# Optimization experiments

Hardware: AMD Instinct MI355X
Metric: run time of the kernel (lower is better)

Reference implementation:

```python
import jax, jax.numpy as jnp
import numpy as np
from jax import lax

B = 1024
T = 32           # length_sec = 384 // (2*2*3*1)
HGT = 7          # height_image = 28 // (1*2*2*1)
CC = 32          # last conv channels
AD = HGT * CC    # abstract_dim = 224
HID = 256        # attention decoder hidden
VOCAB = 29
OUT_LEN = 25


def setup_inputs() -> dict:
    ks = jax.random.split(jax.random.key(0), 24)
    n = lambda k, s, sc=1.0: jax.random.normal(k, s, jnp.float32) * sc
    return {
        "x": n(ks[0], (B, 1, 384, 28)),
        "conv1_w": n(ks[1], (4, 1, 3, 3), 0.2),   "conv1_b": n(ks[2], (4,), 0.1),
        "conv2_w": n(ks[3], (16, 4, 3, 3), 0.2),  "conv2_b": n(ks[4], (16,), 0.1),
        "conv3_w": n(ks[5], (16, 16, 3, 3), 0.2), "conv3_b": n(ks[6], (16,), 0.1),
        "conv4_w": n(ks[7], (32, 16, 3, 3), 0.2), "conv4_b": n(ks[8], (32,), 0.1),
        "h0": n(ks[9], (1, AD)), "c0": n(ks[10], (1, AD)),
        "lstm_Wih": n(ks[11], (4 * AD, AD), 0.05), "lstm_Whh": n(ks[12], (4 * AD, AD), 0.05),
        "lstm_bih": n(ks[13], (4 * AD,), 0.05),    "lstm_bhh": n(ks[14], (4 * AD,), 0.05),
        "att_w": n(ks[15], (1, HID + AD), 0.05),   "att_b": n(ks[16], (1,), 0.05),
        "dec_Wih": n(ks[17], (4 * HID, AD), 0.05), "dec_Whh": n(ks[18], (4 * HID, HID), 0.05),
        "dec_bih": n(ks[19], (4 * HID,), 0.05),    "dec_bhh": n(ks[20], (4 * HID,), 0.05),
        "out_w": n(ks[21], (VOCAB, HID), 0.05),    "out_b": n(ks[22], (VOCAB,), 0.05),
    }


def _lstm_cell(h, c, xt, Wih, Whh, bih, bhh):
    # PyTorch gate order: i, f, g, o
    g = xt @ Wih.T + bih + h @ Whh.T + bhh
    i, f, gg, o = jnp.split(g, 4, axis=-1)
    c = jax.nn.sigmoid(f) * c + jax.nn.sigmoid(i) * jnp.tanh(gg)
    h = jax.nn.sigmoid(o) * jnp.tanh(c)
    return h, c


def reference(x, conv1_w, conv1_b, conv2_w, conv2_b, conv3_w, conv3_b, conv4_w, conv4_b,
              h0, c0, lstm_Wih, lstm_Whh, lstm_bih, lstm_bhh,
              att_w, att_b, dec_Wih, dec_Whh, dec_bih, dec_bhh, out_w, out_b):
    def crp(z, w, b, pool):
        y = lax.conv_general_dilated(z, w, (1, 1), [(1, 1), (1, 1)],
                                     dimension_numbers=('NCHW', 'OIHW', 'NCHW'))
        y = jax.nn.relu(y + b[None, :, None, None])
        win = (1, 1) + pool
        return lax.reduce_window(y, -jnp.inf, lax.max, win, win, 'VALID')

    y1 = crp(x, conv1_w, conv1_b, (2, 1))
    y2 = crp(y1, conv2_w, conv2_b, (2, 2))
    y3 = crp(y2, conv3_w, conv3_b, (3, 2))
    y4 = crp(y3, conv4_w, conv4_b, (1, 1))          # [B, 32, 32, 7]
    Bsz = x.shape[0]
    # y5[b,t,i] = y4[b, i%32, t, i//32]  ==  transpose + reshape (replaces python loop)
    y5 = jnp.transpose(y4, (0, 2, 3, 1)).reshape(Bsz, T, AD)   # [B, T, 224]

    # encoder LSTM (seq-major scan, like torch LSTM)
    def estep(carry, xt):
        h, c = carry
        h, c = _lstm_cell(h, c, xt, lstm_Wih, lstm_Whh, lstm_bih, lstm_bhh)
        return (h, c), h
    h0b = jnp.tile(h0, (Bsz, 1))
    c0b = jnp.tile(c0, (Bsz, 1))
    _, hs = lax.scan(estep, (h0b, c0b), jnp.transpose(y5, (1, 0, 2)))
    y8 = jnp.transpose(hs, (1, 0, 2))                # [B, T, 224]

    # attention decoder: additive score softmax(linear(concat(h, enc)))
    w_h = att_w[0, :HID]     # hidden part
    w_e = att_w[0, HID:]     # encoder part
    enc_score = y8 @ w_e     # [B, T], precomputed once

    def dstep(carry, _):
        h, c = carry
        scores = enc_score + (h @ w_h)[:, None] + att_b[0]      # [B, T]
        alpha = jax.nn.softmax(scores, axis=1)
        ctx = jnp.einsum('bt,btd->bd', alpha, y8)               # [B, 224]
        h, c = _lstm_cell(h, c, ctx, dec_Wih, dec_Whh, dec_bih, dec_bhh)
        return (h, c), h @ out_w.T + out_b                      # [B, 29]

    hdec = jnp.zeros((Bsz, HID), x.dtype)
    _, outs = lax.scan(dstep, (hdec, hdec), None, length=OUT_LEN)  # [25, B, 29]
    return jnp.transpose(outs, (1, 2, 0))            # [B, 29, 25]
```

## Files before the change

### kernel.cpp

```cpp
#include <hip/hip_runtime.h>

typedef unsigned short u16;
typedef unsigned int u32;
typedef unsigned long long u64;
typedef __bf16 bfrag __attribute__((ext_vector_type(8)));
typedef float v4f __attribute__((ext_vector_type(4)));

#define DI __device__ __forceinline__

DI float bf2f(u16 b){ union{u32 u; float f;} c; c.u = ((u32)b)<<16; return c.f; }
DI u16 f2bf(float f){ union{float f; u32 u;} c; c.f=f; u32 u=c.u; return (u16)((u + 0x7FFFu + ((u>>16)&1u))>>16); }
DI float sigm(float x){ return 1.0f/(1.0f+__expf(-x)); }
DI float tanhf_(float x){ float a=fabsf(x); float e=__expf(2.0f*a); float r=1.0f-2.0f/(e+1.0f); return x<0.0f? -r : r; }

DI void cvt_one(const float* __restrict__ src, u16* __restrict__ hi, u16* __restrict__ lo, u32 i){
  float v = src[i]; u16 h = f2bf(v); hi[i] = h; lo[i] = f2bf(v - bf2f(h));
}
__global__ __launch_bounds__(256) void k_cvt4(const float* __restrict__ s0, u16* __restrict__ h0p, u16* __restrict__ l0p,
                                              const float* __restrict__ s1, u16* __restrict__ h1p, u16* __restrict__ l1p,
                                              const float* __restrict__ s2, u16* __restrict__ h2p, u16* __restrict__ l2p,
                                              const float* __restrict__ s3, u16* __restrict__ h3p, u16* __restrict__ l3p,
                                              u32* __restrict__ ef){
  u32 b = blockIdx.x, tid = threadIdx.x;
  if (b < 784u)            cvt_one(s0, h0p, l0p, b*256u + tid);
  else if (b < 1568u)      cvt_one(s1, h1p, l1p, (b-784u)*256u + tid);
  else if (b < 2464u)      cvt_one(s2, h2p, l2p, (b-1568u)*256u + tid);
  else if (b < 3488u)      cvt_one(s3, h3p, l3p, (b-2464u)*256u + tid);
  else {
    #pragma unroll
    for (int j=0;j<4;j++) ef[(u32)j*256u + tid] = 0u;
  }
}

__global__ __launch_bounds__(256) void k_conv1(const float* __restrict__ x, const float* __restrict__ w,
                                               const float* __restrict__ bias, float* __restrict__ y1q, u32 bbase){
  u32 gid = blockIdx.x*256u + threadIdx.x;
  u32 bl = gid/768u, r = gid - bl*768u;
  u32 oy = r>>2, xg = r&3u;
  const float* xb = x + (u64)(bbase+bl)*10752u;
  float win[4][9];
  #pragma unroll
  for (int rr=0; rr<4; rr++){
    int iy = 2*(int)oy - 1 + rr;
    bool vy = (u32)iy < 384u;
    #pragma unroll
    for (int cc=0; cc<9; cc++){
      int ix = (int)(xg*7u) + cc - 1;
      win[rr][cc] = (vy && (u32)ix < 28u) ? xb[iy*28 + ix] : 0.0f;
    }
  }
  #pragma unroll
  for (int co=0; co<4; co++){
    float wf[9];
    #pragma unroll
    for (int j=0;j<9;j++) wf[j] = w[co*9+j];
    float bc = bias[co];
    float* outp = y1q + ((u64)(bl*4u+co)*192u + oy)*28u + xg*7u;
    #pragma unroll
    for (int ox=0; ox<7; ox++){
      float m = 0.0f;
      #pragma unroll
      for (int py=0; py<2; py++){
        float s = bc;
        #pragma unroll
        for (int dy=0; dy<3; dy++)
          #pragma unroll
          for (int dx=0; dx<3; dx++)
            s += win[py+dy][ox+dx]*wf[dy*3+dx];
        m = fmaxf(m, s);
      }
      outp[ox] = m;
    }
  }
}

__global__ __launch_bounds__(256) void k_conv2(const float* __restrict__ y1q, const float* __restrict__ w,
                                               const float* __restrict__ bias, float* __restrict__ y2q){
  u32 gid = blockIdx.x*256u + threadIdx.x;
  u32 bl = gid/1536u, r = gid - bl*1536u;
  u32 oy = r>>4, xg = (r>>3)&1u, cp = r&7u;
  const float* inb = y1q + (u64)bl*21504u;
  float acc[2][7][4];
  #pragma unroll
  for (int c2=0;c2<2;c2++)
    #pragma unroll
    for (int i=0;i<7;i++){ acc[c2][i][0]=0.f;acc[c2][i][1]=0.f;acc[c2][i][2]=0.f;acc[c2][i][3]=0.f; }
  for (int ci=0; ci<4; ci++){
    float win[4][16];
    const float* pl = inb + ci*5376;
    #pragma unroll
    for (int rr=0; rr<4; rr++){
      int iy = 2*(int)oy - 1 + rr;
      bool vy = (u32)iy < 192u;
      #pragma unroll
      for (int cc=0; cc<16; cc++){
        int ix = (int)(xg*14u) + cc - 1;
        win[rr][cc] = (vy && (u32)ix<28u) ? pl[iy*28+ix] : 0.0f;
      }
    }
    float wf[2][9];
    #pragma unroll
    for (int c2=0;c2<2;c2++)
      #pragma unroll
      for (int j=0;j<9;j++) wf[c2][j] = w[((cp*2u+(u32)c2)*4u+(u32)ci)*9u+j];
    #pragma unroll
    for (int c2=0;c2<2;c2++)
      #pragma unroll
      for (int ol=0; ol<7; ol++)
        #pragma unroll
        for (int py=0; py<2; py++)
          #pragma unroll
          for (int px=0; px<2; px++){
            float s = acc[c2][ol][py*2+px];
            #pragma unroll
            for (int dy=0; dy<3; dy++)
              #pragma unroll
              for (int dx=0; dx<3; dx++)
                s += win[py+dy][2*ol+px+dx]*wf[c2][dy*3+dx];
            acc[c2][ol][py*2+px] = s;
          }
  }
  #pragma unroll
  for (int c2=0;c2<2;c2++){
    u32 co = cp*2u+(u32)c2;
    float bc = bias[co];
    float* outp = y2q + ((u64)(bl*16u+co)*96u + oy)*14u + xg*7u;
    #pragma unroll
    for (int ol=0; ol<7; ol++){
      float m = fmaxf(fmaxf(acc[c2][ol][0],acc[c2][ol][1]), fmaxf(acc[c2][ol][2],acc[c2][ol][3])) + bc;
      outp[ol] = fmaxf(m, 0.0f);
    }
  }
}

__global__ __launch_bounds__(256) void k_conv3(const float* __restrict__ y2q, const float* __restrict__ w,
                                               const float* __restrict__ bias, float* __restrict__ y3, u32 bbase){
  u32 gid = blockIdx.x*256u + threadIdx.x;
  u32 bl = gid/512u, r = gid - bl*512u;
  u32 oy = r>>4, co = r&15u;
  const float* inb = y2q + (u64)bl*21504u;
  float acc[7][6];
  #pragma unroll
  for (int i=0;i<7;i++){
    #pragma unroll
    for (int j=0;j<6;j++) acc[i][j]=0.0f;
  }
  for (int ci=0; ci<16; ci++){
    float win[5][16];
    const float* pl = inb + ci*1344;
    #pragma unroll
    for (int rr=0; rr<5; rr++){
      int iy = 3*(int)oy - 1 + rr;
      bool vy = (u32)iy < 96u;
      #pragma unroll
      for (int cc=0; cc<16; cc++){
        int ix = cc-1;
        win[rr][cc] = (vy && (u32)ix<14u) ? pl[iy*14+ix] : 0.0f;
      }
    }
    float wf[9];
    #pragma unroll
    for (int j=0;j<9;j++) wf[j] = w[((u32)co*16u+(u32)ci)*9u+j];
    #pragma unroll
    for (int ox=0; ox<7; ox++){
      #pragma unroll
      for (int py=0; py<3; py++)
        #pragma unroll
        for (int px=0; px<2; px++){
          float s = acc[ox][py*2+px];
          #pragma unroll
          for (int dy=0; dy<3; dy++)
            #pragma unroll
            for (int dx=0; dx<3; dx++)
              s += win[py+dy][2*ox+px+dx]*wf[dy*3+dx];
          acc[ox][py*2+px] = s;
        }
    }
  }
  float bc = bias[co];
  float* outp = y3 + ((u64)((bbase+bl)*16u+co)*32u + oy)*7u;
  #pragma unroll
  for (int ox=0; ox<7; ox++){
    float m = acc[ox][0];
    #pragma unroll
    for (int j=1;j<6;j++) m = fmaxf(m, acc[ox][j]);
    outp[ox] = fmaxf(m + bc, 0.0f);
  }
}

__global__ __launch_bounds__(256) void k_conv4(const float* __restrict__ y3, const float* __restrict__ w,
                                               const float* __restrict__ bias, float* __restrict__ y5){
  u32 gid = blockIdx.x*256u + threadIdx.x;
  u32 b = gid/512u, r = gid - b*512u;
  u32 oy = r>>4, cp = r&15u;
  u32 co0 = cp*2u;
  const float* inb = y3 + (u64)b*3584u;
  float acc[2][7];
  #pragma unroll
  for (int i=0;i<2;i++){
    #pragma unroll
    for (int j=0;j<7;j++) acc[i][j]=0.0f;
  }
  for (int ci=0; ci<16; ci++){
    float win[3][9];
    const float* pl = inb + ci*224;
    #pragma unroll
    for (int rr=0; rr<3; rr++){
      int iy = (int)oy - 1 + rr;
      bool vy = (u32)iy < 32u;
      #pragma unroll
      for (int cc=0; cc<9; cc++){
        int ix = cc-1;
        win[rr][cc] = (vy && (u32)ix<7u) ? pl[iy*7+ix] : 0.0f;
      }
    }
    #pragma unroll
    for (int c2=0; c2<2; c2++){
      float wf[9];
      #pragma unroll
      for (int j=0;j<9;j++) wf[j] = w[((co0+(u32)c2)*16u+(u32)ci)*9u+j];
      #pragma unroll
      for (int ox=0; ox<7; ox++){
        float s = acc[c2][ox];
        #pragma unroll
        for (int dy=0; dy<3; dy++)
          #pragma unroll
          for (int dx=0; dx<3; dx++)
            s += win[dy][ox+dx]*wf[dy*3+dx];
        acc[c2][ox] = s;
      }
    }
  }
  #pragma unroll
  for (int c2=0; c2<2; c2++){
    float bc = bias[co0+(u32)c2];
    #pragma unroll
    for (int ox=0; ox<7; ox++)
      y5[((u64)b*32u + oy)*224u + (u32)ox*32u + (co0+(u32)c2)] = fmaxf(acc[c2][ox] + bc, 0.0f);
  }
}

__global__ __launch_bounds__(1024) void k_zero(u32* __restrict__ p){
  p[threadIdx.x] = 0u;
}

__global__ __launch_bounds__(512, 4) void k_enc7(const u16* __restrict__ WihHi, const u16* __restrict__ WihLo,
                                                 const u16* __restrict__ WhhHi, const u16* __restrict__ WhhLo,
                                                 const float* __restrict__ bih, const float* __restrict__ bhh,
                                                 const float* __restrict__ y5, const float* __restrict__ h0,
                                                 const float* __restrict__ c0, float* __restrict__ y8,
                                                 u32* __restrict__ eflags){
  __shared__ __align__(16) u16 Ahi[16*456], Alo[16*456];
  __shared__ __align__(16) float gsh[16*132];
  __shared__ __align__(16) float bsh[128];
  u32 tid = threadIdx.x, w = tid>>6, lane = tid&63u, nl = lane&15u, quad = lane>>4;
  u32 bid = blockIdx.x, g = bid & 63u, q = bid >> 6;
  u32 b0 = g*16u, hc0 = q*32u;
  if (tid < 128u){
    u32 gi = tid>>5, col = gi*224u + hc0 + (tid&31u);
    bsh[tid] = bih[col] + bhh[col];
  }
  for (u32 it=tid; it<3584u; it+=512u){
    u32 r = it/224u, c = it - r*224u;
    float v = h0[c]; u16 hb = f2bf(v);
    Ahi[r*456u+224u+c] = hb; Alo[r*456u+224u+c] = f2bf(v - bf2f(hb));
  }
  float creg = c0[hc0 + (tid&31u)];
  u32* fE = eflags + g*16u;
  const u32 col = (w>>1)*224u + hc0 + (w&1u)*16u + nl;
  const u32 gl  = (w>>1)*32u  + (w&1u)*16u + nl;
  __syncthreads();
  for (u32 t=0; t<32u; t++){
    #pragma unroll
    for (int i=0;i<7;i++){
      u32 item = (u32)i*512u + tid;
      u32 r = item/224u, c = item - r*224u;
      float v = y5[((u64)(b0+r)*32u + t)*224u + c];
      u16 hb = f2bf(v);
      Ahi[r*456u+c] = hb; Alo[r*456u+c] = f2bf(v - bf2f(hb));
    }
    __syncthreads();
    v4f acc = {};
    #pragma unroll
    for (int kt=0; kt<14; kt++){
      u32 ka = (u32)kt*32u + quad*8u;
      bfrag ah = *(const bfrag*)&Ahi[nl*456u + ka];
      bfrag al = *(const bfrag*)&Alo[nl*456u + ka];
      bfrag bh, bl;
      if (kt<7){
        u64 o = (u64)col*224u + ka;
        bh = *(const bfrag*)&WihHi[o]; bl = *(const bfrag*)&WihLo[o];
      } else {
        u64 o = (u64)col*224u + (ka - 224u);
        bh = *(const bfrag*)&WhhHi[o]; bl = *(const bfrag*)&WhhLo[o];
      }
      acc = __builtin_amdgcn_mfma_f32_16x16x32_bf16(ah, bh, acc, 0,0,0);
      acc = __builtin_amdgcn_mfma_f32_16x16x32_bf16(al, bh, acc, 0,0,0);
      acc = __builtin_amdgcn_mfma_f32_16x16x32_bf16(ah, bl, acc, 0,0,0);
    }
    #pragma unroll
    for (int rg=0; rg<4; rg++)
      gsh[(quad*4u+(u32)rg)*132u + gl] = acc[rg];
    __syncthreads();
    {
      u32 row = tid>>5, hl = tid&31u;
      float gi_ = gsh[row*132u +       hl] + bsh[hl];
      float gf_ = gsh[row*132u + 32u + hl] + bsh[32u+hl];
      float gg_ = gsh[row*132u + 64u + hl] + bsh[64u+hl];
      float go_ = gsh[row*132u + 96u + hl] + bsh[96u+hl];
      float cv = sigm(gf_)*creg + sigm(gi_)*tanhf_(gg_);
      float hv = sigm(go_)*tanhf_(cv);
      creg = cv;
      union{float f; u32 u;} cu; cu.f = hv;
      __hip_atomic_store((u32*)&y8[((u64)(b0+row)*32u + t)*224u + hc0 + hl], cu.u,
                         __ATOMIC_RELAXED, __HIP_MEMORY_SCOPE_AGENT);
    }
    __syncthreads();
    if (tid==0u)
      __hip_atomic_fetch_add(fE, 1u, __ATOMIC_RELEASE, __HIP_MEMORY_SCOPE_AGENT);
    if (t < 31u){
      if (tid==0u){
        while (__hip_atomic_load(fE, __ATOMIC_RELAXED, __HIP_MEMORY_SCOPE_AGENT) < 7u*(t+1u))
          __builtin_amdgcn_s_sleep(2);
      }
      __syncthreads();
      for (u32 it=tid; it<3584u; it+=512u){
        u32 r = it/224u, c = it - r*224u;
        u32 uv = __hip_atomic_load((const u32*)&y8[((u64)(b0+r)*32u + t)*224u + c],
                                   __ATOMIC_RELAXED, __HIP_MEMORY_SCOPE_AGENT);
        union{u32 u; float f;} cu; cu.u = uv;
        u16 hb = f2bf(cu.f);
        Ahi[r*456u+224u+c] = hb; Alo[r*456u+224u+c] = f2bf(cu.f - bf2f(hb));
      }
    }
  }
}

__global__ __launch_bounds__(512) void k_dec4(const float* __restrict__ y8,
    const float* __restrict__ attw, const float* __restrict__ attb,
    const u16* __restrict__ WihHi, const u16* __restrict__ WihLo,
    const u16* __restrict__ WhhHi, const u16* __restrict__ WhhLo,
    const float* __restrict__ bih, const float* __restrict__ bhh,
    u32* __restrict__ hist, u32* __restrict__ ctxc, u32* __restrict__ flags){
  __shared__ __align__(16) u16 Ahi[16*488], Alo[16*488];
  __shared__ __align__(16) float hfull[16*256];
  __shared__ __align__(16) float gsh[16*260];
  __shared__ __align__(16) float esc[16*33];
  __shared__ __align__(16) float alp[16*33];
  __shared__ __align__(16) float bsh[256];
  u32 tid=threadIdx.x, w=tid>>6, lane=tid&63u, nl=lane&15u, quad=lane>>4;
  u32 p = blockIdx.x, xcd = p&7u, slot = p>>3;
  u32 q = xcd>>1;
  u32 g = (xcd&1u)*32u + slot;
  u32 b0 = g*16u, hc0 = q*64u;
  for (u32 it=tid; it<256u; it+=512u){
    u32 gi = it>>6, col = gi*256u + hc0 + (it&63u);
    bsh[it] = bih[col] + bhh[col];
  }
  for (u32 it=tid; it<4096u; it+=512u){
    u32 r=it>>8, c=it&255u;
    Ahi[r*488u+224u+c]=0; Alo[r*488u+224u+c]=0;
    hfull[it]=0.0f;
  }
  {
    u32 r=tid>>5, t=tid&31u;
    const float* yr = y8 + ((u64)(b0+r)*32u + t)*224u;
    const float* we = attw + 256;
    float sacc=0.0f;
    #pragma unroll 8
    for (int j=0;j<224;j++) sacc += yr[j]*we[j];
    esc[r*33u+t] = sacc + attb[0];
  }
  float cst[2] = {0.0f, 0.0f};
  u32* fh = flags + g*16u;
  u32* fc = flags + g*16u + 8u;
  const u32 nt0 = w, nt1 = w + 8u;
  const u32 col0 = (nt0>>2)*256u + hc0 + (nt0&3u)*16u + nl;
  const u32 col1 = (nt1>>2)*256u + hc0 + (nt1&3u)*16u + nl;
  const u32 gl0  = (nt0>>2)*64u + (nt0&3u)*16u + nl;
  const u32 gl1  = (nt1>>2)*64u + (nt1&3u)*16u + nl;
  __syncthreads();
  for (u32 s=0; s<25u; s++){
    if (s>0u){
      if (tid==0u){
        while (__hip_atomic_load(fh, __ATOMIC_RELAXED, __HIP_MEMORY_SCOPE_AGENT) < 4u*s)
          __builtin_amdgcn_s_sleep(2);
      }
      __syncthreads();
      u32* hrow = hist + ((u64)(s-1u)*1024u + b0)*256u;
      for (u32 it=tid; it<4096u; it+=512u){
        u32 v = __hip_atomic_load(&hrow[it], __ATOMIC_RELAXED, __HIP_MEMORY_SCOPE_AGENT);
        u32 r = it>>8, c = it&255u;
        u16 hb = (u16)(v>>16), lb = (u16)(v&0xFFFFu);
        Ahi[r*488u+224u+c] = hb; Alo[r*488u+224u+c] = lb;
        hfull[it] = bf2f(hb) + bf2f(lb);
      }
      __syncthreads();
    }
    {
      u32 r=tid>>5, t=tid&31u;
      float part=0.0f;
      if (s>0u){
        #pragma unroll
        for (int qq=0; qq<8; qq++){
          u32 c = t + (u32)qq*32u;
          part += hfull[r*256u+c]*attw[c];
        }
        #pragma unroll
        for (int off=16; off; off>>=1) part += __shfl_xor(part, off, 32);
      }
      float sv = esc[r*33u+t] + part;
      float mx = sv;
      #pragma unroll
      for (int off=16; off; off>>=1) mx = fmaxf(mx, __shfl_xor(mx, off, 32));
      float e = __expf(sv-mx);
      float ssum = e;
      #pragma unroll
      for (int off=16; off; off>>=1) ssum += __shfl_xor(ssum, off, 32);
      alp[r*33u+t] = e/ssum;
    }
    __syncthreads();
    u32* cdst = ctxc + (u64)(s&1u)*229376u + (u64)g*3584u;
    for (u32 it=tid; it<896u; it+=512u){
      u32 rr = it/56u, cc = it - rr*56u + q*56u;
      const float* yb = y8 + (u64)(b0+rr)*32u*224u + cc;
      float a0=0.0f;
      #pragma unroll
      for (int tt=0; tt<32; tt++) a0 += alp[rr*33u+(u32)tt]*yb[(u32)tt*224u];
      u16 hb = f2bf(a0), lb = f2bf(a0 - bf2f(hb));
      __hip_atomic_store(&cdst[rr*224u+cc], ((u32)hb<<16)|(u32)lb, __ATOMIC_RELAXED, __HIP_MEMORY_SCOPE_AGENT);
    }
    __syncthreads();
    if (tid==0u){
      __hip_atomic_fetch_add(fc, 1u, __ATOMIC_RELEASE, __HIP_MEMORY_SCOPE_AGENT);
      while (__hip_atomic_load(fc, __ATOMIC_RELAXED, __HIP_MEMORY_SCOPE_AGENT) < 4u*(s+1u))
        __builtin_amdgcn_s_sleep(2);
    }
    __syncthreads();
    for (u32 it=tid; it<3584u; it+=512u){
      u32 v = __hip_atomic_load(&cdst[it], __ATOMIC_RELAXED, __HIP_MEMORY_SCOPE_AGENT);
      u32 rr = it/224u, cc = it - rr*224u;
      Ahi[rr*488u+cc] = (u16)(v>>16); Alo[rr*488u+cc] = (u16)(v&0xFFFFu);
    }
    __syncthreads();
    v4f acc0 = {}, acc1 = {};
    #pragma unroll
    for (int kt=0; kt<15; kt++){
      u32 ka = (u32)kt*32u + quad*8u;
      bfrag afh = *(const bfrag*)&Ahi[nl*488u + ka];
      bfrag afl = *(const bfrag*)&Alo[nl*488u + ka];
      bfrag b0h, b0l, b1h, b1l;
      if (kt<7){
        u64 o0 = (u64)col0*224u + ka, o1 = (u64)col1*224u + ka;
        b0h = *(const bfrag*)&WihHi[o0]; b0l = *(const bfrag*)&WihLo[o0];
        b1h = *(const bfrag*)&WihHi[o1]; b1l = *(const bfrag*)&WihLo[o1];
      } else {
        u32 kb = ka - 224u;
        u64 o0 = (u64)col0*256u + kb, o1 = (u64)col1*256u + kb;
        b0h = *(const bfrag*)&WhhHi[o0]; b0l = *(const bfrag*)&WhhLo[o0];
        b1h = *(const bfrag*)&WhhHi[o1]; b1l = *(const bfrag*)&WhhLo[o1];
      }
      acc0 = __builtin_amdgcn_mfma_f32_16x16x32_bf16(afh, b0h, acc0, 0,0,0);
      acc0 = __builtin_amdgcn_mfma_f32_16x16x32_bf16(afl, b0h, acc0, 0,0,0);
      acc0 = __builtin_amdgcn_mfma_f32_16x16x32_bf16(afh, b0l, acc0, 0,0,0);
      acc1 = __builtin_amdgcn_mfma_f32_16x16x32_bf16(afh, b1h, acc1, 0,0,0);
      acc1 = __builtin_amdgcn_mfma_f32_16x16x32_bf16(afl, b1h, acc1, 0,0,0);
      acc1 = __builtin_amdgcn_mfma_f32_16x16x32_bf16(afh, b1l, acc1, 0,0,0);
    }
    #pragma unroll
    for (int rg=0; rg<4; rg++){
      gsh[(quad*4u+(u32)rg)*260u + gl0] = acc0[rg];
      gsh[(quad*4u+(u32)rg)*260u + gl1] = acc1[rg];
    }
    __syncthreads();
    u32* hdst = hist + ((u64)s*1024u + b0)*256u + hc0;
    #pragma unroll
    for (int k2=0; k2<2; k2++){
      u32 l = (u32)k2*512u + tid;
      u32 row = l>>6, hl = l&63u;
      float gi_ = gsh[row*260u + hl]         + bsh[hl];
      float gf_ = gsh[row*260u + 64u  + hl]  + bsh[64u+hl];
      float gg_ = gsh[row*260u + 128u + hl]  + bsh[128u+hl];
      float go_ = gsh[row*260u + 192u + hl]  + bsh[192u+hl];
      float cv = sigm(gf_)*cst[k2] + sigm(gi_)*tanhf_(gg_);
      float hv = sigm(go_)*tanhf_(cv);
      cst[k2] = cv;
      u16 hb = f2bf(hv), lb = f2bf(hv - bf2f(hb));
      __hip_atomic_store(&hdst[row*256u + hl], ((u32)hb<<16)|(u32)lb, __ATOMIC_RELAXED, __HIP_MEMORY_SCOPE_AGENT);
    }
    __syncthreads();
    if (tid==0u)
      __hip_atomic_fetch_add(fh, 1u, __ATOMIC_RELEASE, __HIP_MEMORY_SCOPE_AGENT);
  }
}

__global__ __launch_bounds__(256) void k_out(const u32* __restrict__ hist, const float* __restrict__ outw,
                                             const float* __restrict__ outb, float* __restrict__ outp){
  __shared__ __align__(16) float wsh[29*260];
  __shared__ __align__(16) float hrow[256];
  u32 tid = threadIdx.x, b = blockIdx.x;
  for (u32 it=tid; it<7424u; it+=256u){
    u32 v = it/256u, c = it&255u;
    wsh[v*260u+c] = outw[v*256u+c];
  }
  __syncthreads();
  for (u32 s=0; s<25u; s++){
    u32 v = hist[((u64)s*1024u + b)*256u + tid];
    hrow[tid] = bf2f((u16)(v>>16)) + bf2f((u16)(v&0xFFFFu));
    __syncthreads();
    if (tid < 232u){
      u32 vv = tid>>3, k8 = tid&7u;
      float a = 0.0f;
      #pragma unroll
      for (int j=0;j<32;j++) a += hrow[k8*32u+(u32)j]*wsh[vv*260u + k8*32u + (u32)j];
      #pragma unroll
      for (int off=4; off; off>>=1) a += __shfl_xor(a, off, 8);
      if (k8==0u) outp[((u64)b*29u + vv)*25u + s] = a + outb[vv];
    }
    __syncthreads();
  }
}

extern "C" void kernel_launch(void* const* d_in, const int* in_sizes, int n_in,
                              void* d_out, int out_size, void* d_ws, size_t ws_size,
                              hipStream_t stream){
  (void)in_sizes; (void)n_in; (void)out_size; (void)ws_size;
  const float* x    = (const float*)d_in[0];
  const float* c1w  = (const float*)d_in[1];
  const float* c1b  = (const float*)d_in[2];
  const float* c2w  = (const float*)d_in[3];
  const float* c2b  = (const float*)d_in[4];
  const float* c3w  = (const float*)d_in[5];
  const float* c3b  = (const float*)d_in[6];
  const float* c4w  = (const float*)d_in[7];
  const float* c4b  = (const float*)d_in[8];
  const float* h0   = (const float*)d_in[9];
  const float* c0   = (const float*)d_in[10];
  const float* lWih = (const float*)d_in[11];
  const float* lWhh = (const float*)d_in[12];
  const float* lbih = (const float*)d_in[13];
  const float* lbhh = (const float*)d_in[14];
  const float* attw = (const float*)d_in[15];
  const float* attb = (const float*)d_in[16];
  const float* dWih = (const float*)d_in[17];
  const float* dWhh = (const float*)d_in[18];
  const float* dbih = (const float*)d_in[19];
  const float* dbhh = (const float*)d_in[20];
  const float* outw = (const float*)d_in[21];
  const float* outb = (const float*)d_in[22];
  float* out = (float*)d_out;
  char* ws = (char*)d_ws;
  float* y1q = (float*)(ws);
  float* y2q = (float*)(ws + 22020096ull);
  float* y3  = (float*)(ws + 44040192ull);
  float* y5  = (float*)(ws);
  float* y8  = (float*)(ws + 29360128ull);
  u32* hist  = (u32*)(ws);
  u32* ctxc  = (u32*)(ws + 26214400ull);
  u32* flags = (u32*)(ws + 28049408ull);
  u16* lWihHi = (u16*)(ws + 58720256ull);
  u16* lWihLo = (u16*)(ws + 59121664ull);
  u16* lWhhHi = (u16*)(ws + 59523072ull);
  u16* lWhhLo = (u16*)(ws + 59924480ull);
  u16* dWihHi = (u16*)(ws + 60325888ull);
  u16* dWihLo = (u16*)(ws + 60784640ull);
  u16* dWhhHi = (u16*)(ws + 61243392ull);
  u16* dWhhLo = (u16*)(ws + 61767680ull);
  u32* eflags = (u32*)d_out;

  k_cvt4<<<dim3(3489), dim3(256), 0, stream>>>(lWih, lWihHi, lWihLo,
                                               lWhh, lWhhHi, lWhhLo,
                                               dWih, dWihHi, dWihLo,
                                               dWhh, dWhhHi, dWhhLo, eflags);
  for (u32 q=0; q<4; q++){
    k_conv1<<<dim3(768),  dim3(256), 0, stream>>>(x, c1w, c1b, y1q, q*256u);
    k_conv2<<<dim3(1536), dim3(256), 0, stream>>>(y1q, c2w, c2b, y2q);
    k_conv3<<<dim3(512),  dim3(256), 0, stream>>>(y2q, c3w, c3b, y3, q*256u);
  }
  k_conv4<<<dim3(2048), dim3(256), 0, stream>>>(y3, c4w, c4b, y5);
  k_enc7 <<<dim3(448), dim3(512), 0, stream>>>(lWihHi, lWihLo, lWhhHi, lWhhLo, lbih, lbhh,
                                               y5, h0, c0, y8, eflags);
  k_zero <<<dim3(1), dim3(1024), 0, stream>>>(flags);
  k_dec4 <<<dim3(256), dim3(512), 0, stream>>>(y8, attw, attb, dWihHi, dWihLo, dWhhHi, dWhhLo,
                                               dbih, dbhh, hist, ctxc, flags);
  k_out  <<<dim3(1024), dim3(256), 0, stream>>>(hist, outw, outb, out);
}
```

Baseline: 2.009 ms.

## Fuse four conv-relu-pool stages into one per-sample kernel using LDS

Replaces the four separate conv kernels, which were launched per quarter batch, with a single kernel where each block handles one sample. Intermediate activations and all conv weights are kept in shared memory, and conv1/conv2 are processed in row strips. This removes the large global round-trips of intermediate activations and most kernel launches. In exchange, the large shared-memory footprint limits each CU to one 256-thread block, reducing latency hiding, and conv1/conv2 now use scalar shared-memory loops with per-element bounds checks.

Result: slower. 4.446 ms (+121.3%).

```diff
diff --git a/kernel.cpp b/kernel.cpp
--- a/kernel.cpp
+++ b/kernel.cpp
@@ -32,211 +32,177 @@
   }
 }
 
-__global__ __launch_bounds__(256) void k_conv1(const float* __restrict__ x, const float* __restrict__ w,
-                                               const float* __restrict__ bias, float* __restrict__ y1q, u32 bbase){
-  u32 gid = blockIdx.x*256u + threadIdx.x;
-  u32 bl = gid/768u, r = gid - bl*768u;
-  u32 oy = r>>2, xg = r&3u;
-  const float* xb = x + (u64)(bbase+bl)*10752u;
-  float win[4][9];
-  #pragma unroll
-  for (int rr=0; rr<4; rr++){
-    int iy = 2*(int)oy - 1 + rr;
-    bool vy = (u32)iy < 384u;
-    #pragma unroll
-    for (int cc=0; cc<9; cc++){
-      int ix = (int)(xg*7u) + cc - 1;
-      win[rr][cc] = (vy && (u32)ix < 28u) ? xb[iy*28 + ix] : 0.0f;
-    }
-  }
-  #pragma unroll
-  for (int co=0; co<4; co++){
-    float wf[9];
-    #pragma unroll
-    for (int j=0;j<9;j++) wf[j] = w[co*9+j];
-    float bc = bias[co];
-    float* outp = y1q + ((u64)(bl*4u+co)*192u + oy)*28u + xg*7u;
-    #pragma unroll
-    for (int ox=0; ox<7; ox++){
+__global__ __launch_bounds__(256, 1) void k_convf(const float* __restrict__ x,
+    const float* __restrict__ c1w, const float* __restrict__ c1b,
+    const float* __restrict__ c2w, const float* __restrict__ c2b,
+    const float* __restrict__ c3w, const float* __restrict__ c3b,
+    const float* __restrict__ c4w, const float* __restrict__ c4b,
+    float* __restrict__ y5){
+  __shared__ __align__(16) float wsh[7592];
+  __shared__ __align__(16) float y2s[21504];
+  __shared__ __align__(16) float y1s[2016];
+  __shared__ __align__(16) float y3s[3584];
+  u32 tid = threadIdx.x, b = blockIdx.x;
+  const float* xb = x + (u64)b*10752u;
+  for (u32 it=tid; it<576u;  it+=256u) wsh[it]        = c2w[it];
+  for (u32 it=tid; it<2304u; it+=256u) wsh[576u+it]   = c3w[it];
+  for (u32 it=tid; it<4608u; it+=256u) wsh[2880u+it]  = c4w[it];
+  if (tid < 36u) wsh[7556u+tid] = c1w[tid];
+  if (tid < 4u)  wsh[7488u+tid] = c1b[tid];
+  if (tid < 16u) wsh[7492u+tid] = c2b[tid];
+  if (tid < 16u) wsh[7508u+tid] = c3b[tid];
+  if (tid < 32u) wsh[7524u+tid] = c4b[tid];
+  __syncthreads();
+  for (u32 s=0; s<12u; s++){
+    for (u32 it=tid; it<2016u; it+=256u){
+      u32 ch = it/504u, rem = it - ch*504u;
+      u32 j = rem/28u, c = rem - j*28u;
+      int gr = 16*(int)s - 1 + (int)j;
       float m = 0.0f;
-      #pragma unroll
-      for (int py=0; py<2; py++){
-        float s = bc;
-        #pragma unroll
-        for (int dy=0; dy<3; dy++)
+      if ((u32)gr < 192u){
+        float bc = wsh[7488u+ch];
+        #pragma unroll
+        for (int py=0; py<2; py++){
+          float a = bc;
           #pragma unroll
-          for (int dx=0; dx<3; dx++)
-            s += win[py+dy][ox+dx]*wf[dy*3+dx];
-        m = fmaxf(m, s);
-      }
-      outp[ox] = m;
-    }
-  }
-}
-
-__global__ __launch_bounds__(256) void k_conv2(const float* __restrict__ y1q, const float* __restrict__ w,
-                                               const float* __restrict__ bias, float* __restrict__ y2q){
-  u32 gid = blockIdx.x*256u + threadIdx.x;
-  u32 bl = gid/1536u, r = gid - bl*1536u;
-  u32 oy = r>>4, xg = (r>>3)&1u, cp = r&7u;
-  const float* inb = y1q + (u64)bl*21504u;
-  float acc[2][7][4];
-  #pragma unroll
-  for (int c2=0;c2<2;c2++)
-    #pragma unroll
-    for (int i=0;i<7;i++){ acc[c2][i][0]=0.f;acc[c2][i][1]=0.f;acc[c2][i][2]=0.f;acc[c2][i][3]=0.f; }
-  for (int ci=0; ci<4; ci++){
-    float win[4][16];
-    const float* pl = inb + ci*5376;
-    #pragma unroll
-    for (int rr=0; rr<4; rr++){
-      int iy = 2*(int)oy - 1 + rr;
-      bool vy = (u32)iy < 192u;
-      #pragma unroll
-      for (int cc=0; cc<16; cc++){
-        int ix = (int)(xg*14u) + cc - 1;
-        win[rr][cc] = (vy && (u32)ix<28u) ? pl[iy*28+ix] : 0.0f;
-      }
-    }
-    float wf[2][9];
-    #pragma unroll
-    for (int c2=0;c2<2;c2++)
-      #pragma unroll
-      for (int j=0;j<9;j++) wf[c2][j] = w[((cp*2u+(u32)c2)*4u+(u32)ci)*9u+j];
-    #pragma unroll
-    for (int c2=0;c2<2;c2++)
-      #pragma unroll
-      for (int ol=0; ol<7; ol++)
+          for (int dy=0; dy<3; dy++){
+            int iy = 2*gr + py - 1 + dy;
+            bool vy = (u32)iy < 384u;
+            #pragma unroll
+            for (int dx=0; dx<3; dx++){
+              int ix = (int)c - 1 + dx;
+              a += (vy && (u32)ix < 28u) ? xb[iy*28+ix]*wsh[7556u+ch*9u+(u32)(dy*3+dx)] : 0.0f;
+            }
+          }
+          m = fmaxf(m, a);
+        }
+      }
+      y1s[it] = m;
+    }
+    __syncthreads();
+    for (u32 it=tid; it<1792u; it+=256u){
+      u32 co = it/112u, rem = it - co*112u;
+      u32 r = rem/14u, ox = rem - r*14u;
+      float a0=0.f, a1=0.f, a2=0.f, a3=0.f;
+      #pragma unroll
+      for (int ci=0; ci<4; ci++){
+        const float* wp = &wsh[(co*4u+(u32)ci)*9u];
         #pragma unroll
         for (int py=0; py<2; py++)
           #pragma unroll
           for (int px=0; px<2; px++){
-            float s = acc[c2][ol][py*2+px];
+            float sacc = (py==0) ? (px==0 ? a0 : a1) : (px==0 ? a2 : a3);
+            #pragma unroll
+            for (int dy=0; dy<3; dy++){
+              u32 lr = 2u*r + (u32)(py+dy);
+              #pragma unroll
+              for (int dx=0; dx<3; dx++){
+                int lc = 2*(int)ox + px - 1 + dx;
+                sacc += ((u32)lc < 28u) ? y1s[(u32)ci*504u + lr*28u + (u32)lc]*wp[dy*3+dx] : 0.0f;
+              }
+            }
+            if (py==0){ if (px==0) a0=sacc; else a1=sacc; } else { if (px==0) a2=sacc; else a3=sacc; }
+          }
+      }
+      float m = fmaxf(fmaxf(a0,a1), fmaxf(a2,a3)) + wsh[7492u+co];
+      y2s[co*1344u + (8u*s+r)*14u + ox] = fmaxf(m, 0.0f);
+    }
+    __syncthreads();
+  }
+  for (u32 it=tid; it<512u; it+=256u){
+    u32 co = it>>5, oy = it&31u;
+    float acc[7][6];
+    #pragma unroll
+    for (int i=0;i<7;i++){
+      #pragma unroll
+      for (int j=0;j<6;j++) acc[i][j]=0.0f;
+    }
+    for (int ci=0; ci<16; ci++){
+      float win[5][16];
+      #pragma unroll
+      for (int rr=0; rr<5; rr++){
+        int iy = 3*(int)oy - 1 + rr;
+        bool vy = (u32)iy < 96u;
+        #pragma unroll
+        for (int cc=0; cc<16; cc++){
+          int ix = cc-1;
+          win[rr][cc] = (vy && (u32)ix<14u) ? y2s[(u32)ci*1344u + (u32)iy*14u + (u32)ix] : 0.0f;
+        }
+      }
+      float wf[9];
+      #pragma unroll
+      for (int j=0;j<9;j++) wf[j] = wsh[576u + (co*16u+(u32)ci)*9u + (u32)j];
+      #pragma unroll
+      for (int ox=0; ox<7; ox++){
+        #pragma unroll
+        for (int py=0; py<3; py++)
+          #pragma unroll
+          for (int px=0; px<2; px++){
+            float sacc = acc[ox][py*2+px];
             #pragma unroll
             for (int dy=0; dy<3; dy++)
               #pragma unroll
               for (int dx=0; dx<3; dx++)
-                s += win[py+dy][2*ol+px+dx]*wf[c2][dy*3+dx];
-            acc[c2][ol][py*2+px] = s;
+                sacc += win[py+dy][2*ox+px+dx]*wf[dy*3+dx];
+            acc[ox][py*2+px] = sacc;
           }
-  }
-  #pragma unroll
-  for (int c2=0;c2<2;c2++){
-    u32 co = cp*2u+(u32)c2;
-    float bc = bias[co];
-    float* outp = y2q + ((u64)(bl*16u+co)*96u + oy)*14u + xg*7u;
-    #pragma unroll
-    for (int ol=0; ol<7; ol++){
-      float m = fmaxf(fmaxf(acc[c2][ol][0],acc[c2][ol][1]), fmaxf(acc[c2][ol][2],acc[c2][ol][3])) + bc;
-      outp[ol] = fmaxf(m, 0.0f);
-    }
-  }
-}
-
-__global__ __launch_bounds__(256) void k_conv3(const float* __restrict__ y2q, const float* __restrict__ w,
-                                               const float* __restrict__ bias, float* __restrict__ y3, u32 bbase){
-  u32 gid = blockIdx.x*256u + threadIdx.x;
-  u32 bl = gid/512u, r = gid - bl*512u;
-  u32 oy = r>>4, co = r&15u;
-  const float* inb = y2q + (u64)bl*21504u;
-  float acc[7][6];
-  #pragma unroll
-  for (int i=0;i<7;i++){
-    #pragma unroll
-    for (int j=0;j<6;j++) acc[i][j]=0.0f;
-  }
-  for (int ci=0; ci<16; ci++){
-    float win[5][16];
-    const float* pl = inb + ci*1344;
-    #pragma unroll
-    for (int rr=0; rr<5; rr++){
-      int iy = 3*(int)oy - 1 + rr;
-      bool vy = (u32)iy < 96u;
-      #pragma unroll
-      for (int cc=0; cc<16; cc++){
-        int ix = cc-1;
-        win[rr][cc] = (vy && (u32)ix<14u) ? pl[iy*14+ix] : 0.0f;
-      }
-    }
-    float wf[9];
-    #pragma unroll
-    for (int j=0;j<9;j++) wf[j] = w[((u32)co*16u+(u32)ci)*9u+j];
+      }
+    }
+    float bc = wsh[7508u+co];
     #pragma unroll
     for (int ox=0; ox<7; ox++){
-      #pragma unroll
-      for (int py=0; py<3; py++)
-        #pragma unroll
-        for (int px=0; px<2; px++){
-          float s = acc[ox][py*2+px];
+      float m = acc[ox][0];
+      #pragma unroll
+      for (int j=1;j<6;j++) m = fmaxf(m, acc[ox][j]);
+      y3s[co*224u + oy*7u + (u32)ox] = fmaxf(m + bc, 0.0f);
+    }
+  }
+  __syncthreads();
+  for (u32 it=tid; it<512u; it+=256u){
+    u32 oy = it>>4, cp = it&15u;
+    u32 co0 = cp*2u;
+    float acc[2][7];
+    #pragma unroll
+    for (int i=0;i<2;i++){
+      #pragma unroll
+      for (int j=0;j<7;j++) acc[i][j]=0.0f;
+    }
+    for (int ci=0; ci<16; ci++){
+      float win[3][9];
+      #pragma unroll
+      for (int rr=0; rr<3; rr++){
+        int iy = (int)oy - 1 + rr;
+        bool vy = (u32)iy < 32u;
+        #pragma unroll
+        for (int cc=0; cc<9; cc++){
+          int ix = cc-1;
+          win[rr][cc] = (vy && (u32)ix<7u) ? y3s[(u32)ci*224u + (u32)iy*7u + (u32)ix] : 0.0f;
+        }
+      }
+      #pragma unroll
+      for (int c2=0; c2<2; c2++){
+        float wf[9];
+        #pragma unroll
+        for (int j=0;j<9;j++) wf[j] = wsh[2880u + ((co0+(u32)c2)*16u+(u32)ci)*9u + (u32)j];
+        #pragma unroll
+        for (int ox=0; ox<7; ox++){
+          float sacc = acc[c2][ox];
           #pragma unroll
           for (int dy=0; dy<3; dy++)
             #pragma unroll
             for (int dx=0; dx<3; dx++)
-              s += win[py+dy][2*ox+px+dx]*wf[dy*3+dx];
-          acc[ox][py*2+px] = s;
+              sacc += win[dy][ox+dx]*wf[dy*3+dx];
+          acc[c2][ox] = sacc;
         }
-    }
-  }
-  float bc = bias[co];
-  float* outp = y3 + ((u64)((bbase+bl)*16u+co)*32u + oy)*7u;
-  #pragma unroll
-  for (int ox=0; ox<7; ox++){
-    float m = acc[ox][0];
-    #pragma unroll
-    for (int j=1;j<6;j++) m = fmaxf(m, acc[ox][j]);
-    outp[ox] = fmaxf(m + bc, 0.0f);
-  }
-}
-
-__global__ __launch_bounds__(256) void k_conv4(const float* __restrict__ y3, const float* __restrict__ w,
-                                               const float* __restrict__ bias, float* __restrict__ y5){
-  u32 gid = blockIdx.x*256u + threadIdx.x;
-  u32 b = gid/512u, r = gid - b*512u;
-  u32 oy = r>>4, cp = r&15u;
-  u32 co0 = cp*2u;
-  const float* inb = y3 + (u64)b*3584u;
-  float acc[2][7];
-  #pragma unroll
-  for (int i=0;i<2;i++){
-    #pragma unroll
-    for (int j=0;j<7;j++) acc[i][j]=0.0f;
-  }
-  for (int ci=0; ci<16; ci++){
-    float win[3][9];
-    const float* pl = inb + ci*224;
-    #pragma unroll
-    for (int rr=0; rr<3; rr++){
-      int iy = (int)oy - 1 + rr;
-      bool vy = (u32)iy < 32u;
-      #pragma unroll
-      for (int cc=0; cc<9; cc++){
-        int ix = cc-1;
-        win[rr][cc] = (vy && (u32)ix<7u) ? pl[iy*7+ix] : 0.0f;
       }
     }
     #pragma unroll
     for (int c2=0; c2<2; c2++){
-      float wf[9];
-      #pragma unroll
-      for (int j=0;j<9;j++) wf[j] = w[((co0+(u32)c2)*16u+(u32)ci)*9u+j];
-      #pragma unroll
-      for (int ox=0; ox<7; ox++){
-        float s = acc[c2][ox];
-        #pragma unroll
-        for (int dy=0; dy<3; dy++)
-          #pragma unroll
-          for (int dx=0; dx<3; dx++)
-            s += win[dy][ox+dx]*wf[dy*3+dx];
-        acc[c2][ox] = s;
-      }
-    }
-  }
-  #pragma unroll
-  for (int c2=0; c2<2; c2++){
-    float bc = bias[co0+(u32)c2];
-    #pragma unroll
-    for (int ox=0; ox<7; ox++)
-      y5[((u64)b*32u + oy)*224u + (u32)ox*32u + (co0+(u32)c2)] = fmaxf(acc[c2][ox] + bc, 0.0f);
+      float bc = wsh[7524u+co0+(u32)c2];
+      #pragma unroll
+      for (int ox=0; ox<7; ox++)
+        y5[((u64)b*32u + oy)*224u + (u32)ox*32u + (co0+(u32)c2)] = fmaxf(acc[c2][ox] + bc, 0.0f);
+    }
   }
 }
 
@@ -550,9 +516,6 @@
   const float* outb = (const float*)d_in[22];
   float* out = (float*)d_out;
   char* ws = (char*)d_ws;
-  float* y1q = (float*)(ws);
-  float* y2q = (float*)(ws + 22020096ull);
-  float* y3  = (float*)(ws + 44040192ull);
   float* y5  = (float*)(ws);
   float* y8  = (float*)(ws + 29360128ull);
   u32* hist  = (u32*)(ws);
@@ -572,12 +535,7 @@
                                                lWhh, lWhhHi, lWhhLo,
                                                dWih, dWihHi, dWihLo,
                                                dWhh, dWhhHi, dWhhLo, eflags);
-  for (u32 q=0; q<4; q++){
-    k_conv1<<<dim3(768),  dim3(256), 0, stream>>>(x, c1w, c1b, y1q, q*256u);
-    k_conv2<<<dim3(1536), dim3(256), 0, stream>>>(y1q, c2w, c2b, y2q);
-    k_conv3<<<dim3(512),  dim3(256), 0, stream>>>(y2q, c3w, c3b, y3, q*256u);
-  }
-  k_conv4<<<dim3(2048), dim3(256), 0, stream>>>(y3, c4w, c4b, y5);
+  k_convf<<<dim3(1024), dim3(256), 0, stream>>>(x, c1w, c1b, c2w, c2b, c3w, c3b, c4w, c4b, y5);
   k_enc7 <<<dim3(448), dim3(512), 0, stream>>>(lWihHi, lWihLo, lWhhHi, lWhhLo, lbih, lbhh,
                                                y5, h0, c0, y8, eflags);
   k_zero <<<dim3(1), dim3(1024), 0, stream>>>(flags);
```
